# Optimization experiments

Measured on AMD Instinct MI355X. Metric: run time of the kernel, lower is better.

Reference implementation:

```python
import jax, jax.numpy as jnp
import numpy as np

K = (0.3, 0.3, 0.4)   # args.args_k_0..2
EPS = 1e-8


def squash(v, axis=-1):
    norm = jnp.linalg.norm(v, axis=axis, keepdims=True)
    scale = norm ** 2 / (1.0 + norm ** 2) / (norm + EPS)
    return scale * v


def setup_inputs() -> dict:
    key = jax.random.key(0)
    kx, kw = jax.random.split(key)
    B, IN, DIN, OUT, DOUT = 128, 4608, 8, 10, 16
    x = jax.random.normal(kx, (B, IN, DIN), dtype=jnp.float32)
    weight = 0.1 * jax.random.normal(kw, (OUT, IN, DOUT, DIN), dtype=jnp.float32)
    return {"x": x, "weight": weight}


def reference(x, weight):
    # x: [B, I, Din], weight: [O, I, Dout, Din]
    # x_hat[b,o,i,d] = sum_k weight[o,i,d,k] * x[b,i,k]
    x_hat = jnp.einsum('oidk,bik->boid', weight, x)  # [B, O, I, Dout]
    x_hat_d = jax.lax.stop_gradient(x_hat)
    B, O, I, D = x_hat.shape
    b = jnp.zeros((B, O, I), dtype=x.dtype)
    feats = []
    for it in range(3):
        c = jax.nn.softmax(b, axis=1)[..., None]          # [B, O, I, 1], softmax over out caps
        if it == 2:
            out = squash(jnp.sum(c * x_hat, axis=-2, keepdims=True))      # [B, O, 1, D]
        else:
            out = squash(jnp.sum(c * x_hat_d, axis=-2, keepdims=True))    # [B, O, 1, D]
            b = b + jnp.sum(out * x_hat_d, axis=-1)                       # agreement update
        feats.append(out * K[it])
    # stack -> [3, B, O, 1, D]; squeeze caps-sum axis; sum over iterations
    outputs = jnp.sum(jnp.squeeze(jnp.stack(feats), axis=-2), axis=0)     # [B, O, D]
    return outputs.reshape(B, O, 4, 4)
```

## Files before the change

### kernel.cpp

```cpp
#include <hip/hip_runtime.h>

#define B_    128
#define I_    4608
#define O_    10
#define D_    16
#define NCHUNKS 2304
#define NIB   64
#define CPB   36
#define CHH   5120
#define PSET  20480

typedef _Float16 f16x2 __attribute__((ext_vector_type(2)));
typedef _Float16 f16x4 __attribute__((ext_vector_type(4)));
typedef _Float16 f16x8 __attribute__((ext_vector_type(8)));
typedef float    f32x4 __attribute__((ext_vector_type(4)));
typedef __fp16   pk16x2 __attribute__((ext_vector_type(2)));
typedef unsigned int uint2v __attribute__((ext_vector_type(2)));

__device__ __forceinline__ f16x4 pack4(float a, float b, float c, float d) {
    union { f16x4 v; pk16x2 p[2]; } u;
    u.p[0] = __builtin_amdgcn_cvt_pkrtz(a, b);
    u.p[1] = __builtin_amdgcn_cvt_pkrtz(c, d);
    return u.v;
}
__device__ __forceinline__ f16x2 splat_h2(float a) {
    union { f16x2 v; pk16x2 p; } u;
    u.p = __builtin_amdgcn_cvt_pkrtz(a, a);
    return u.v;
}

__global__ __launch_bounds__(256)
void prep_kernel(const float* __restrict__ w, _Float16* __restrict__ pw)
{
    __shared__ float wch[2560];
    const int c = blockIdx.x, t = threadIdx.x;
#pragma unroll
    for (int o = 0; o < O_; ++o)
        wch[o * 256 + t] = w[(long)o * (I_ * 128) + (long)c * 256 + t];
    __syncthreads();

    _Float16* dst = pw + (long)c * CHH;
#pragma unroll
    for (int kk = 0; kk < 5; ++kk) {
        const int sidx = t + kk * 256;
        const int hg   = sidx & 1;
        const int lane = (sidx >> 1) & 63;
        const int pi   = sidx >> 7;
        const int p    = pi % 5;
        const int img  = pi / 5;
        const int r = lane & 15, g = lane >> 4;
        const int o = 2 * p + hg;
        f16x4 val;
        if (img == 1) {
            const float4 gg = *(const float4*)&wch[o * 256 + (g & 1) * 128 + r * 8 + (g >> 1) * 4];
            val = pack4(gg.x, gg.y, gg.z, gg.w);
        } else {
            const int bofs = o * 256 + ((r >> 2) & 1) * 128 + (r >> 3) * 4 + (r & 3);
            val = pack4(wch[bofs + (g * 4 + 0) * 8], wch[bofs + (g * 4 + 1) * 8],
                        wch[bofs + (g * 4 + 2) * 8], wch[bofs + (g * 4 + 3) * 8]);
        }
        *(f16x4*)(dst + (long)sidx * 4) = val;
    }
}

template<int MODE>
__global__ __launch_bounds__(512, 4)
void pass_kernel(const float* __restrict__ x,
                 const _Float16* __restrict__ pw,
                 const float* __restrict__ v,
                 float* __restrict__ parts)
{
    __shared__ float red[4 * 2560];

    const int tid  = threadIdx.x;
    const int lane = tid & 63;
    const int wv   = tid >> 6;
    const int bl   = lane & 15;
    const int g    = lane >> 4;
    const int u    = blockIdx.x;
    const int xcd  = u & 7, s = u >> 3;
    const int ib   = xcd * 8 + (s & 7);
    const int bg   = s >> 3;
    const int c0   = ib * CPB;
    const int cend = c0 + CPB;
    const int iloc = g & 1, kq = g >> 1;
    const int b0   = bg * 16 + bl;

    f16x4 vf[O_];
    if (MODE == 1) {
#pragma unroll
        for (int o = 0; o < O_; ++o) {
            const float4 vv = *(const float4*)(v + ((long)b0 * O_ + o) * D_ + g * 4);
            vf[o] = pack4(vv.x, vv.y, vv.z, vv.w);
        }
    }

    f32x4 S[O_];
#pragma unroll
    for (int o = 0; o < O_; ++o) S[o] = (f32x4)(0.f);

    const long lofs = (long)lane * 8;
    auto fragp = [&](int c, int img, int p) {
        return (const f16x8*)(pw + (long)c * CHH + img * 2560 + p * 512 + lofs);
    };
    auto xp = [&](int c) {
        return (const float4*)(x + ((long)b0 * I_ + 2 * c + iloc) * 8 + kq * 4);
    };

    int c = c0 + wv;
    f16x8 f0[5], f1[5];
    float4 xqC, xqN;
    if (MODE == 1) {
#pragma unroll
        for (int p = 0; p < 5; ++p) f0[p] = *fragp(c, 0, p);
    }
#pragma unroll
    for (int p = 0; p < 5; ++p) f1[p] = *fragp(c, 1, p);
    xqC = *xp(c);

#pragma unroll
    for (int t5 = 0; t5 < 5; ++t5) {
        const bool valid = (c < cend);
        int cn = c + 8; if (cn > NCHUNKS - 1) cn = NCHUNKS - 1;
        if (valid) {
            xqN = *xp(cn);

            float cs[O_];
            if (MODE == 1) {
#pragma unroll
                for (int p = 0; p < 5; ++p) {
                    f16x4 ae, ao;
                    ae[0]=f0[p][0]; ae[1]=f0[p][1]; ae[2]=f0[p][2]; ae[3]=f0[p][3];
                    ao[0]=f0[p][4]; ao[1]=f0[p][5]; ao[2]=f0[p][6]; ao[3]=f0[p][7];
                    const f32x4 ua = __builtin_amdgcn_mfma_f32_16x16x16f16(ae, vf[2*p],   (f32x4)(0.f), 0, 0, 0);
                    const f32x4 ub = __builtin_amdgcn_mfma_f32_16x16x16f16(ao, vf[2*p+1], (f32x4)(0.f), 0, 0, 0);
                    float d0 = ua[0] * xqC.x; d0 = fmaf(ua[1], xqC.y, d0);
                    d0 = fmaf(ua[2], xqC.z, d0); d0 = fmaf(ua[3], xqC.w, d0);
                    float d1 = ub[0] * xqC.x; d1 = fmaf(ub[1], xqC.y, d1);
                    d1 = fmaf(ub[2], xqC.z, d1); d1 = fmaf(ub[3], xqC.w, d1);
                    cs[2*p] = d0; cs[2*p+1] = d1;
                }
#pragma unroll
                for (int p = 0; p < 5; ++p) f0[p] = *fragp(cn, 0, p);
                float ssum = 0.f;
#pragma unroll
                for (int o = 0; o < O_; ++o) {
                    const unsigned int tt = __float_as_uint(cs[o]);
                    const uint2v sw = __builtin_amdgcn_permlane32_swap(tt, tt, false, false);
                    const float e = __expf(__uint_as_float(sw[0]) + __uint_as_float(sw[1]));
                    cs[o] = e; ssum += e;
                }
                const float inv = 1.f / ssum;
#pragma unroll
                for (int o = 0; o < O_; ++o) cs[o] *= inv;
            }

            union F4 { f16x4 v; f16x2 h[2]; };
            F4 xh;
            xh.v = pack4(xqC.x, xqC.y, xqC.z, xqC.w);
#pragma unroll
            for (int p = 0; p < 5; ++p) {
                f16x4 pe, po;
                pe[0]=f1[p][0]; pe[1]=f1[p][1]; pe[2]=f1[p][2]; pe[3]=f1[p][3];
                po[0]=f1[p][4]; po[1]=f1[p][5]; po[2]=f1[p][6]; po[3]=f1[p][7];
                F4 ye, yo;
                if (MODE == 0) { ye = xh; yo = xh; }
                else {
                    const f16x2 ce = splat_h2(cs[2*p]);
                    const f16x2 co = splat_h2(cs[2*p+1]);
                    ye.h[0] = xh.h[0] * ce; ye.h[1] = xh.h[1] * ce;
                    yo.h[0] = xh.h[0] * co; yo.h[1] = xh.h[1] * co;
                }
                S[2*p]   = __builtin_amdgcn_mfma_f32_16x16x16f16(pe, ye.v, S[2*p],   0, 0, 0);
                S[2*p+1] = __builtin_amdgcn_mfma_f32_16x16x16f16(po, yo.v, S[2*p+1], 0, 0, 0);
            }
#pragma unroll
            for (int p = 0; p < 5; ++p) f1[p] = *fragp(cn, 1, p);
            xqC = xqN;
        }
        c += 8;
    }

    auto slot = [&](int w, int o) {
        return &red[w * 2560 + o * 256 + lane * 4];
    };
#define TREE_WR(WSRC)                                                       \
    if (wv >= WSRC && wv < 2 * WSRC) {                                      \
        _Pragma("unroll") for (int o = 0; o < O_; ++o)                      \
            *(f32x4*)slot(wv - WSRC, o) = S[o];                             \
    }                                                                       \
    __syncthreads();                                                        \
    if (wv < WSRC) {                                                        \
        _Pragma("unroll") for (int o = 0; o < O_; ++o)                      \
            S[o] += *(f32x4*)slot(wv, o);                                   \
    }                                                                       \
    __syncthreads();

    TREE_WR(4)
    TREE_WR(2)
    TREE_WR(1)
#undef TREE_WR

    if (wv == 0) {
#pragma unroll
        for (int o = 0; o < O_; ++o) {
            float* pp = parts + (long)ib * PSET + ((long)b0 * O_ + o) * D_ + g * 4;
            *(f32x4*)pp = S[o];
        }
    }
}

__global__ __launch_bounds__(256)
void reduce_squash(const float* __restrict__ parts, float* __restrict__ v_buf,
                   float* __restrict__ out, float kscale, float pre, int mode)
{
    __shared__ float red2[4][16];
    const int tid  = threadIdx.x;
    const int lane = tid & 63;
    const int wv   = tid >> 6;
    const int g2   = blockIdx.x;
    const int pg   = tid >> 4;
    const int d    = tid & 15;

    float s = 0.f;
#pragma unroll
    for (int k = 0; k < 4; ++k)
        s += parts[(long)(pg * 4 + k) * PSET + g2 * D_ + d];

    s += __shfl_xor(s, 16);
    s += __shfl_xor(s, 32);
    if (lane < 16) red2[wv][lane] = s;
    __syncthreads();

    if (tid < 16) {
        float tot = (red2[0][tid] + red2[1][tid]) + (red2[2][tid] + red2[3][tid]);
        tot *= pre;
        float n2 = tot * tot;
        n2 += __shfl_xor(n2, 1);
        n2 += __shfl_xor(n2, 2);
        n2 += __shfl_xor(n2, 4);
        n2 += __shfl_xor(n2, 8);
        const float n     = sqrtf(n2);
        const float scale = n2 / ((1.f + n2) * (n + 1e-8f));
        const float o_    = scale * tot;
        const int idx = g2 * D_ + tid;
        if (mode == 0)      { v_buf[idx] = o_;  out[idx]  = kscale * o_; }
        else if (mode == 1) { v_buf[idx] += o_; out[idx] += kscale * o_; }
        else                {                   out[idx] += kscale * o_; }
    }
}

extern "C" void kernel_launch(void* const* d_in, const int* in_sizes, int n_in,
                              void* d_out, int out_size, void* d_ws, size_t ws_size,
                              hipStream_t stream)
{
    const float* x = (const float*)d_in[0];
    const float* w = (const float*)d_in[1];
    float* out   = (float*)d_out;
    float* parts = (float*)d_ws;
    float* v_buf = parts + (long)NIB * PSET;
    _Float16* pw = (_Float16*)(v_buf + B_ * O_ * D_);

    prep_kernel<<<NCHUNKS, 256, 0, stream>>>(w, pw);

    pass_kernel<0><<<512, 512, 0, stream>>>(x, pw, v_buf, parts);
    reduce_squash<<<1280, 256, 0, stream>>>(parts, v_buf, out, 0.3f, 0.1f, 0);

    pass_kernel<1><<<512, 512, 0, stream>>>(x, pw, v_buf, parts);
    reduce_squash<<<1280, 256, 0, stream>>>(parts, v_buf, out, 0.3f, 1.0f, 1);

    pass_kernel<1><<<512, 512, 0, stream>>>(x, pw, v_buf, parts);
    reduce_squash<<<1280, 256, 0, stream>>>(parts, v_buf, out, 0.4f, 1.0f, 2);
}
```

Before: 71.22 us.

## Share weight chunks across batch waves via LDS double buffering in pass kernel

Reorganizes the pass kernel so each block covers all 128 batch rows (8 waves × 16) over a 9-chunk input slice, instead of each wave walking its own chunks for 16 batch rows. Weight fragments are staged into a double-buffered LDS tile with global_load_lds and shared by all waves. The in-block tree reduction goes away because each wave owns distinct batch rows, and partial sums rise to 256 per output, which reduce_squash now sums. This is meant to cut redundant global weight traffic and the reduction barriers, at the cost of a __syncthreads per chunk, less register prefetch of x, fewer blocks (256) and a larger final reduction.

```diff
diff --git a/kernel.cpp b/kernel.cpp
--- a/kernel.cpp
+++ b/kernel.cpp
@@ -5,8 +5,8 @@
 #define O_    10
 #define D_    16
 #define NCHUNKS 2304
-#define NIB   64
-#define CPB   36
+#define NIB   256
+#define CPB   9
 #define CHH   5120
 #define PSET  20480
 
@@ -27,6 +27,11 @@
     union { f16x2 v; pk16x2 p; } u;
     u.p = __builtin_amdgcn_cvt_pkrtz(a, a);
     return u.v;
+}
+__device__ __forceinline__ void gload_lds16(const _Float16* g, _Float16* l) {
+    __builtin_amdgcn_global_load_lds(
+        (const __attribute__((address_space(1))) void*)g,
+        (__attribute__((address_space(3))) void*)l, 16, 0, 0);
 }
 
 __global__ __launch_bounds__(256)
@@ -64,27 +69,34 @@
 }
 
 template<int MODE>
-__global__ __launch_bounds__(512, 4)
+__global__ __launch_bounds__(512, 2)
 void pass_kernel(const float* __restrict__ x,
                  const _Float16* __restrict__ pw,
                  const float* __restrict__ v,
                  float* __restrict__ parts)
 {
-    __shared__ float red[4 * 2560];
+    __shared__ _Float16 lds[2][CHH];
 
     const int tid  = threadIdx.x;
     const int lane = tid & 63;
     const int wv   = tid >> 6;
     const int bl   = lane & 15;
     const int g    = lane >> 4;
-    const int u    = blockIdx.x;
-    const int xcd  = u & 7, s = u >> 3;
-    const int ib   = xcd * 8 + (s & 7);
-    const int bg   = s >> 3;
+    const int ib   = blockIdx.x;
     const int c0   = ib * CPB;
-    const int cend = c0 + CPB;
     const int iloc = g & 1, kq = g >> 1;
-    const int b0   = bg * 16 + bl;
+    const int b0   = wv * 16 + bl;
+
+    const long srcoff = (MODE == 1) ? 0 : 2560;
+    const int  pofs   = (MODE == 1) ? 2560 : 0;
+    const bool a0 = (MODE == 1) ? true : (tid < 320);
+    const bool a1 = (MODE == 1) && (tid < 128);
+
+    auto stage = [&](int c, int buf) {
+        const _Float16* pc = pw + (long)c * CHH + srcoff;
+        if (a0) gload_lds16(pc + (long)tid * 8, &lds[buf][(long)tid * 8]);
+        if (a1) gload_lds16(pc + (long)(tid + 512) * 8, &lds[buf][(long)(tid + 512) * 8]);
+    };
 
     f16x4 vf[O_];
     if (MODE == 1) {
@@ -99,114 +111,72 @@
 #pragma unroll
     for (int o = 0; o < O_; ++o) S[o] = (f32x4)(0.f);
 
-    const long lofs = (long)lane * 8;
-    auto fragp = [&](int c, int img, int p) {
-        return (const f16x8*)(pw + (long)c * CHH + img * 2560 + p * 512 + lofs);
-    };
-    auto xp = [&](int c) {
-        return (const float4*)(x + ((long)b0 * I_ + 2 * c + iloc) * 8 + kq * 4);
-    };
-
-    int c = c0 + wv;
-    f16x8 f0[5], f1[5];
-    float4 xqC, xqN;
-    if (MODE == 1) {
-#pragma unroll
-        for (int p = 0; p < 5; ++p) f0[p] = *fragp(c, 0, p);
-    }
-#pragma unroll
-    for (int p = 0; p < 5; ++p) f1[p] = *fragp(c, 1, p);
-    xqC = *xp(c);
-
-#pragma unroll
-    for (int t5 = 0; t5 < 5; ++t5) {
-        const bool valid = (c < cend);
-        int cn = c + 8; if (cn > NCHUNKS - 1) cn = NCHUNKS - 1;
-        if (valid) {
-            xqN = *xp(cn);
-
-            float cs[O_];
-            if (MODE == 1) {
-#pragma unroll
-                for (int p = 0; p < 5; ++p) {
-                    f16x4 ae, ao;
-                    ae[0]=f0[p][0]; ae[1]=f0[p][1]; ae[2]=f0[p][2]; ae[3]=f0[p][3];
-                    ao[0]=f0[p][4]; ao[1]=f0[p][5]; ao[2]=f0[p][6]; ao[3]=f0[p][7];
-                    const f32x4 ua = __builtin_amdgcn_mfma_f32_16x16x16f16(ae, vf[2*p],   (f32x4)(0.f), 0, 0, 0);
-                    const f32x4 ub = __builtin_amdgcn_mfma_f32_16x16x16f16(ao, vf[2*p+1], (f32x4)(0.f), 0, 0, 0);
-                    float d0 = ua[0] * xqC.x; d0 = fmaf(ua[1], xqC.y, d0);
-                    d0 = fmaf(ua[2], xqC.z, d0); d0 = fmaf(ua[3], xqC.w, d0);
-                    float d1 = ub[0] * xqC.x; d1 = fmaf(ub[1], xqC.y, d1);
-                    d1 = fmaf(ub[2], xqC.z, d1); d1 = fmaf(ub[3], xqC.w, d1);
-                    cs[2*p] = d0; cs[2*p+1] = d1;
-                }
-#pragma unroll
-                for (int p = 0; p < 5; ++p) f0[p] = *fragp(cn, 0, p);
-                float ssum = 0.f;
-#pragma unroll
-                for (int o = 0; o < O_; ++o) {
-                    const unsigned int tt = __float_as_uint(cs[o]);
-                    const uint2v sw = __builtin_amdgcn_permlane32_swap(tt, tt, false, false);
-                    const float e = __expf(__uint_as_float(sw[0]) + __uint_as_float(sw[1]));
-                    cs[o] = e; ssum += e;
-                }
-                const float inv = 1.f / ssum;
-#pragma unroll
-                for (int o = 0; o < O_; ++o) cs[o] *= inv;
+    stage(c0, 0);
+
+#pragma unroll 1
+    for (int t = 0; t < CPB; ++t) {
+        __syncthreads();
+        if (t + 1 < CPB) stage(c0 + t + 1, (t + 1) & 1);
+
+        const int c = c0 + t;
+        const float4 xq = *(const float4*)(x + ((long)b0 * I_ + 2 * c + iloc) * 8 + kq * 4);
+        const _Float16* base = &lds[t & 1][0];
+
+        float cs[O_];
+        if (MODE == 1) {
+#pragma unroll
+            for (int p = 0; p < 5; ++p) {
+                const f16x8 af = *(const f16x8*)(base + p * 512 + lane * 8);
+                f16x4 ae, ao;
+                ae[0]=af[0]; ae[1]=af[1]; ae[2]=af[2]; ae[3]=af[3];
+                ao[0]=af[4]; ao[1]=af[5]; ao[2]=af[6]; ao[3]=af[7];
+                const f32x4 ua = __builtin_amdgcn_mfma_f32_16x16x16f16(ae, vf[2*p],   (f32x4)(0.f), 0, 0, 0);
+                const f32x4 ub = __builtin_amdgcn_mfma_f32_16x16x16f16(ao, vf[2*p+1], (f32x4)(0.f), 0, 0, 0);
+                float d0 = ua[0] * xq.x; d0 = fmaf(ua[1], xq.y, d0);
+                d0 = fmaf(ua[2], xq.z, d0); d0 = fmaf(ua[3], xq.w, d0);
+                float d1 = ub[0] * xq.x; d1 = fmaf(ub[1], xq.y, d1);
+                d1 = fmaf(ub[2], xq.z, d1); d1 = fmaf(ub[3], xq.w, d1);
+                cs[2*p] = d0; cs[2*p+1] = d1;
             }
-
-            union F4 { f16x4 v; f16x2 h[2]; };
-            F4 xh;
-            xh.v = pack4(xqC.x, xqC.y, xqC.z, xqC.w);
-#pragma unroll
-            for (int p = 0; p < 5; ++p) {
-                f16x4 pe, po;
-                pe[0]=f1[p][0]; pe[1]=f1[p][1]; pe[2]=f1[p][2]; pe[3]=f1[p][3];
-                po[0]=f1[p][4]; po[1]=f1[p][5]; po[2]=f1[p][6]; po[3]=f1[p][7];
-                F4 ye, yo;
-                if (MODE == 0) { ye = xh; yo = xh; }
-                else {
-                    const f16x2 ce = splat_h2(cs[2*p]);
-                    const f16x2 co = splat_h2(cs[2*p+1]);
-                    ye.h[0] = xh.h[0] * ce; ye.h[1] = xh.h[1] * ce;
-                    yo.h[0] = xh.h[0] * co; yo.h[1] = xh.h[1] * co;
-                }
-                S[2*p]   = __builtin_amdgcn_mfma_f32_16x16x16f16(pe, ye.v, S[2*p],   0, 0, 0);
-                S[2*p+1] = __builtin_amdgcn_mfma_f32_16x16x16f16(po, yo.v, S[2*p+1], 0, 0, 0);
+            float ssum = 0.f;
+#pragma unroll
+            for (int o = 0; o < O_; ++o) {
+                const unsigned int tt = __float_as_uint(cs[o]);
+                const uint2v sw = __builtin_amdgcn_permlane32_swap(tt, tt, false, false);
+                const float e = __expf(__uint_as_float(sw[0]) + __uint_as_float(sw[1]));
+                cs[o] = e; ssum += e;
             }
-#pragma unroll
-            for (int p = 0; p < 5; ++p) f1[p] = *fragp(cn, 1, p);
-            xqC = xqN;
-        }
-        c += 8;
-    }
-
-    auto slot = [&](int w, int o) {
-        return &red[w * 2560 + o * 256 + lane * 4];
-    };
-#define TREE_WR(WSRC)                                                       \
-    if (wv >= WSRC && wv < 2 * WSRC) {                                      \
-        _Pragma("unroll") for (int o = 0; o < O_; ++o)                      \
-            *(f32x4*)slot(wv - WSRC, o) = S[o];                             \
-    }                                                                       \
-    __syncthreads();                                                        \
-    if (wv < WSRC) {                                                        \
-        _Pragma("unroll") for (int o = 0; o < O_; ++o)                      \
-            S[o] += *(f32x4*)slot(wv, o);                                   \
-    }                                                                       \
-    __syncthreads();
-
-    TREE_WR(4)
-    TREE_WR(2)
-    TREE_WR(1)
-#undef TREE_WR
-
-    if (wv == 0) {
-#pragma unroll
-        for (int o = 0; o < O_; ++o) {
-            float* pp = parts + (long)ib * PSET + ((long)b0 * O_ + o) * D_ + g * 4;
-            *(f32x4*)pp = S[o];
-        }
+            const float inv = 1.f / ssum;
+#pragma unroll
+            for (int o = 0; o < O_; ++o) cs[o] *= inv;
+        }
+
+        union F4 { f16x4 v; f16x2 h[2]; };
+        F4 xh;
+        xh.v = pack4(xq.x, xq.y, xq.z, xq.w);
+#pragma unroll
+        for (int p = 0; p < 5; ++p) {
+            const f16x8 pf = *(const f16x8*)(base + pofs + p * 512 + lane * 8);
+            f16x4 pe, po;
+            pe[0]=pf[0]; pe[1]=pf[1]; pe[2]=pf[2]; pe[3]=pf[3];
+            po[0]=pf[4]; po[1]=pf[5]; po[2]=pf[6]; po[3]=pf[7];
+            F4 ye, yo;
+            if (MODE == 0) { ye = xh; yo = xh; }
+            else {
+                const f16x2 ce = splat_h2(cs[2*p]);
+                const f16x2 co = splat_h2(cs[2*p+1]);
+                ye.h[0] = xh.h[0] * ce; ye.h[1] = xh.h[1] * ce;
+                yo.h[0] = xh.h[0] * co; yo.h[1] = xh.h[1] * co;
+            }
+            S[2*p]   = __builtin_amdgcn_mfma_f32_16x16x16f16(pe, ye.v, S[2*p],   0, 0, 0);
+            S[2*p+1] = __builtin_amdgcn_mfma_f32_16x16x16f16(po, yo.v, S[2*p+1], 0, 0, 0);
+        }
+    }
+
+#pragma unroll
+    for (int o = 0; o < O_; ++o) {
+        float* pp = parts + (long)ib * PSET + ((long)b0 * O_ + o) * D_ + g * 4;
+        *(f32x4*)pp = S[o];
     }
 }
 
@@ -224,8 +194,8 @@
 
     float s = 0.f;
 #pragma unroll
-    for (int k = 0; k < 4; ++k)
-        s += parts[(long)(pg * 4 + k) * PSET + g2 * D_ + d];
+    for (int k = 0; k < 16; ++k)
+        s += parts[(long)(pg * 16 + k) * PSET + g2 * D_ + d];
 
     s += __shfl_xor(s, 16);
     s += __shfl_xor(s, 32);
@@ -263,12 +233,12 @@
 
     prep_kernel<<<NCHUNKS, 256, 0, stream>>>(w, pw);
 
-    pass_kernel<0><<<512, 512, 0, stream>>>(x, pw, v_buf, parts);
+    pass_kernel<0><<<NIB, 512, 0, stream>>>(x, pw, v_buf, parts);
     reduce_squash<<<1280, 256, 0, stream>>>(parts, v_buf, out, 0.3f, 0.1f, 0);
 
-    pass_kernel<1><<<512, 512, 0, stream>>>(x, pw, v_buf, parts);
+    pass_kernel<1><<<NIB, 512, 0, stream>>>(x, pw, v_buf, parts);
     reduce_squash<<<1280, 256, 0, stream>>>(parts, v_buf, out, 0.3f, 1.0f, 1);
 
-    pass_kernel<1><<<512, 512, 0, stream>>>(x, pw, v_buf, parts);
+    pass_kernel<1><<<NIB, 512, 0, stream>>>(x, pw, v_buf, parts);
     reduce_squash<<<1280, 256, 0, stream>>>(parts, v_buf, out, 0.4f, 1.0f, 2);
 }
```

New measurement: 94.71 us. +33.0%, slower.

## Drop transposed weight copy and derive it in-register via identity MFMA

Applied to the files above, without the earlier changes.

The prepared fp16 weight buffer previously held two layouts per chunk (original and transposed). Now only one layout is stored, which halves weight bytes read by the pass kernels. In MODE 1 the transposed fragment is rebuilt in registers by multiplying with an identity matrix through an extra MFMA, followed by an fp32-to-fp16 repack. This trades memory bandwidth for extra MFMA and conversion work in the routing passes.

```diff
diff --git a/kernel.cpp b/kernel.cpp
--- a/kernel.cpp
+++ b/kernel.cpp
@@ -7,7 +7,7 @@
 #define NCHUNKS 2304
 #define NIB   64
 #define CPB   36
-#define CHH   5120
+#define CHH   2560
 #define PSET  20480
 
 typedef _Float16 f16x2 __attribute__((ext_vector_type(2)));
@@ -41,25 +41,17 @@
 
     _Float16* dst = pw + (long)c * CHH;
 #pragma unroll
-    for (int kk = 0; kk < 5; ++kk) {
+    for (int kk = 0; kk < 3; ++kk) {
         const int sidx = t + kk * 256;
-        const int hg   = sidx & 1;
-        const int lane = (sidx >> 1) & 63;
-        const int pi   = sidx >> 7;
-        const int p    = pi % 5;
-        const int img  = pi / 5;
-        const int r = lane & 15, g = lane >> 4;
-        const int o = 2 * p + hg;
-        f16x4 val;
-        if (img == 1) {
+        if (sidx < 640) {
+            const int hg   = sidx & 1;
+            const int lane = (sidx >> 1) & 63;
+            const int p    = sidx >> 7;
+            const int r = lane & 15, g = lane >> 4;
+            const int o = 2 * p + hg;
             const float4 gg = *(const float4*)&wch[o * 256 + (g & 1) * 128 + r * 8 + (g >> 1) * 4];
-            val = pack4(gg.x, gg.y, gg.z, gg.w);
-        } else {
-            const int bofs = o * 256 + ((r >> 2) & 1) * 128 + (r >> 3) * 4 + (r & 3);
-            val = pack4(wch[bofs + (g * 4 + 0) * 8], wch[bofs + (g * 4 + 1) * 8],
-                        wch[bofs + (g * 4 + 2) * 8], wch[bofs + (g * 4 + 3) * 8]);
-        }
-        *(f16x4*)(dst + (long)sidx * 4) = val;
+            *(f16x4*)(dst + (long)sidx * 4) = pack4(gg.x, gg.y, gg.z, gg.w);
+        }
     }
 }
 
@@ -86,6 +78,10 @@
     const int iloc = g & 1, kq = g >> 1;
     const int b0   = bg * 16 + bl;
 
+    f16x4 idf;
+#pragma unroll
+    for (int j = 0; j < 4; ++j) idf[j] = (_Float16)((bl == 4 * g + j) ? 1.f : 0.f);
+
     f16x4 vf[O_];
     if (MODE == 1) {
 #pragma unroll
@@ -100,22 +96,18 @@
     for (int o = 0; o < O_; ++o) S[o] = (f32x4)(0.f);
 
     const long lofs = (long)lane * 8;
-    auto fragp = [&](int c, int img, int p) {
-        return (const f16x8*)(pw + (long)c * CHH + img * 2560 + p * 512 + lofs);
+    auto fragp = [&](int c, int p) {
+        return (const f16x8*)(pw + (long)c * CHH + p * 512 + lofs);
     };
     auto xp = [&](int c) {
         return (const float4*)(x + ((long)b0 * I_ + 2 * c + iloc) * 8 + kq * 4);
     };
 
     int c = c0 + wv;
-    f16x8 f0[5], f1[5];
+    f16x8 f1[5];
     float4 xqC, xqN;
-    if (MODE == 1) {
-#pragma unroll
-        for (int p = 0; p < 5; ++p) f0[p] = *fragp(c, 0, p);
-    }
-#pragma unroll
-    for (int p = 0; p < 5; ++p) f1[p] = *fragp(c, 1, p);
+#pragma unroll
+    for (int p = 0; p < 5; ++p) f1[p] = *fragp(c, p);
     xqC = *xp(c);
 
 #pragma unroll
@@ -129,9 +121,13 @@
             if (MODE == 1) {
 #pragma unroll
                 for (int p = 0; p < 5; ++p) {
-                    f16x4 ae, ao;
-                    ae[0]=f0[p][0]; ae[1]=f0[p][1]; ae[2]=f0[p][2]; ae[3]=f0[p][3];
-                    ao[0]=f0[p][4]; ao[1]=f0[p][5]; ao[2]=f0[p][6]; ao[3]=f0[p][7];
+                    f16x4 pe, po;
+                    pe[0]=f1[p][0]; pe[1]=f1[p][1]; pe[2]=f1[p][2]; pe[3]=f1[p][3];
+                    po[0]=f1[p][4]; po[1]=f1[p][5]; po[2]=f1[p][6]; po[3]=f1[p][7];
+                    const f32x4 te = __builtin_amdgcn_mfma_f32_16x16x16f16(pe, idf, (f32x4)(0.f), 0, 0, 0);
+                    const f32x4 to = __builtin_amdgcn_mfma_f32_16x16x16f16(po, idf, (f32x4)(0.f), 0, 0, 0);
+                    const f16x4 ae = pack4(te[0], te[1], te[2], te[3]);
+                    const f16x4 ao = pack4(to[0], to[1], to[2], to[3]);
                     const f32x4 ua = __builtin_amdgcn_mfma_f32_16x16x16f16(ae, vf[2*p],   (f32x4)(0.f), 0, 0, 0);
                     const f32x4 ub = __builtin_amdgcn_mfma_f32_16x16x16f16(ao, vf[2*p+1], (f32x4)(0.f), 0, 0, 0);
                     float d0 = ua[0] * xqC.x; d0 = fmaf(ua[1], xqC.y, d0);
@@ -140,8 +136,6 @@
                     d1 = fmaf(ub[2], xqC.z, d1); d1 = fmaf(ub[3], xqC.w, d1);
                     cs[2*p] = d0; cs[2*p+1] = d1;
                 }
-#pragma unroll
-                for (int p = 0; p < 5; ++p) f0[p] = *fragp(cn, 0, p);
                 float ssum = 0.f;
 #pragma unroll
                 for (int o = 0; o < O_; ++o) {
@@ -175,7 +169,7 @@
                 S[2*p+1] = __builtin_amdgcn_mfma_f32_16x16x16f16(po, yo.v, S[2*p+1], 0, 0, 0);
             }
 #pragma unroll
-            for (int p = 0; p < 5; ++p) f1[p] = *fragp(cn, 1, p);
+            for (int p = 0; p < 5; ++p) f1[p] = *fragp(cn, p);
             xqC = xqN;
         }
         c += 8;
```

New measurement: 66.53 us, median of 2. 1.07x faster.
